# Optimization experiments

Measured on AMD Instinct MI355X. Metric: run time of the kernel, lower is better.

The kernel has to match this reference:

```python
import jax, jax.numpy as jnp
import numpy as np

B, L, DIM = 2, 2048, 2048
H, KV, HD = 32, 8, 64
N_REP = H // KV


def setup_inputs() -> dict:
    key = jax.random.key(0)
    ks = jax.random.split(key, 6)
    std = DIM ** -0.5
    std_o = (H * HD) ** -0.5 / np.sqrt(2 * 24)
    x = jax.random.normal(ks[0], (B, L, DIM), dtype=jnp.float32)
    # freqs_cis packs (cos, sin), each [L, head_dim//2]
    pos = jnp.arange(L, dtype=jnp.float32)[:, None]
    inv = 1.0 / (10000.0 ** (jnp.arange(0, HD, 2, dtype=jnp.float32) / HD))
    ang = pos * inv[None, :]
    freqs_cis = jnp.stack([jnp.cos(ang), jnp.sin(ang)], axis=0)
    wq = jax.random.normal(ks[1], (H * HD, DIM), dtype=jnp.float32) * std
    wk = jax.random.normal(ks[2], (KV * HD, DIM), dtype=jnp.float32) * std
    wv = jax.random.normal(ks[3], (KV * HD, DIM), dtype=jnp.float32) * std
    wo = jax.random.normal(ks[4], (DIM, H * HD), dtype=jnp.float32) * std_o
    return {"x": x, "freqs_cis": freqs_cis, "wq": wq, "wk": wk, "wv": wv, "wo": wo}


def _rope(t, cos, sin):
    # t: [B, L, h, HD]; interleaved (real, imag) pairs in last dim
    tr = t.reshape(*t.shape[:-1], HD // 2, 2)
    out_r = tr[..., 0] * cos - tr[..., 1] * sin
    out_i = tr[..., 0] * sin + tr[..., 1] * cos
    return jnp.stack([out_r, out_i], axis=-1).reshape(t.shape)


def reference(x, freqs_cis, wq, wk, wv, wo):
    Bb, Ll, _ = x.shape
    xq = (x @ wq.T).reshape(Bb, Ll, H, HD)
    xk = (x @ wk.T).reshape(Bb, Ll, KV, HD)
    xv = (x @ wv.T).reshape(Bb, Ll, KV, HD)
    cos = freqs_cis[0].reshape(1, Ll, 1, HD // 2)
    sin = freqs_cis[1].reshape(1, Ll, 1, HD // 2)
    xq = _rope(xq, cos, sin)
    xk = _rope(xk, cos, sin)
    # GQA: repeat_interleave kv heads to n_heads
    xk = jnp.repeat(xk, N_REP, axis=2)
    xv = jnp.repeat(xv, N_REP, axis=2)
    scale = 1.0 / jnp.sqrt(jnp.asarray(HD, x.dtype))
    scores = jnp.einsum('bihd,bjhd->bhij', xq, xk) * scale
    causal = jnp.tril(jnp.ones((Ll, Ll), dtype=bool))
    scores = jnp.where(causal[None, None], scores, jnp.finfo(scores.dtype).min)
    attn = jax.nn.softmax(scores, axis=-1)
    out = jnp.einsum('bhij,bjhd->bihd', attn, xv).reshape(Bb, Ll, H * HD)
    return out @ wo.T
```

## Files before the change

### kernel.cpp

```cpp
#include <hip/hip_runtime.h>
#include <stdint.h>

typedef __bf16 bf16;
typedef __attribute__((ext_vector_type(8))) __bf16 bf16x8;
typedef __attribute__((ext_vector_type(4))) __bf16 bf16x4;
typedef __attribute__((ext_vector_type(8))) short short8v;
typedef __attribute__((ext_vector_type(4))) short short4v;
typedef __attribute__((ext_vector_type(4))) float f32x4;

static constexpr int Bn = 2, Ln = 2048, DIMn = 2048, Hn = 32, KVn = 8, HDn = 64;
static constexpr int TS = 3072;

#if defined(__has_builtin)
#if __has_builtin(__builtin_amdgcn_exp2f)
#define EXP2(x) __builtin_amdgcn_exp2f(x)
#endif
#endif
#ifndef EXP2
#define EXP2(x) exp2f(x)
#endif

#define TO_LDS(p) ((__attribute__((address_space(3))) uint32_t*)(uintptr_t)(p))
#define TO_GLB(p) ((const __attribute__((address_space(1))) uint32_t*)(uintptr_t)(p))

__global__ void cast_all(const float* __restrict__ x, const float* __restrict__ wq,
                         const float* __restrict__ wk, const float* __restrict__ wv,
                         const float* __restrict__ wo, bf16* __restrict__ xb,
                         bf16* __restrict__ wqkvb, bf16* __restrict__ wob) {
    size_t i = (size_t)(blockIdx.x * blockDim.x + threadIdx.x) * 4;
    const float* src;
    bf16* dst;
    if (i < 8388608) {
        src = x + i; dst = xb + i;
    } else if (i < 8388608 + 6291456) {
        size_t j = i - 8388608;
        dst = wqkvb + j;
        if (j < 4194304)      src = wq + j;
        else if (j < 5242880) src = wk + (j - 4194304);
        else                  src = wv + (j - 5242880);
    } else {
        size_t j = i - 14680064;
        src = wo + j; dst = wob + j;
    }
    float4 v = *(const float4*)src;
    bf16 o[4] = {(bf16)v.x, (bf16)v.y, (bf16)v.z, (bf16)v.w};
    *(uint64_t*)dst = *(uint64_t*)o;
}

__global__ void rope_k(bf16* __restrict__ qkv, const float* __restrict__ fc) {
    int idx = blockIdx.x * blockDim.x + threadIdx.x;
    int i   = idx & 31;
    int kvh = (idx >> 5) & 7;
    int bl  = idx >> 8;
    int l   = bl & (Ln - 1);
    size_t base = (size_t)bl * TS + 2048 + kvh * 64 + 2 * i;
    float cr = fc[l * 32 + i];
    float sr = fc[65536 + l * 32 + i];
    float x0 = (float)qkv[base], x1 = (float)qkv[base + 1];
    qkv[base]     = (bf16)(x0 * cr - x1 * sr);
    qkv[base + 1] = (bf16)(x0 * sr + x1 * cr);
}

static __device__ __forceinline__ void barrier_f() {
    asm volatile("" ::: "memory");
    __builtin_amdgcn_s_barrier();
    asm volatile("" ::: "memory");
}

template <int N>
static __device__ __forceinline__ void waitcnt_vm() {
    if constexpr (N == 0) asm volatile("s_waitcnt vmcnt(0)" ::: "memory");
    else if constexpr (N == 6) asm volatile("s_waitcnt vmcnt(6)" ::: "memory");
    else if constexpr (N == 7) asm volatile("s_waitcnt vmcnt(7)" ::: "memory");
    else static_assert(N == 0 || N == 6 || N == 7, "add vmcnt literal");
}

template <int BM, int BN, bool OUT_BF16>
__global__ __launch_bounds__(512, 1) void gemm256(const bf16* __restrict__ A,
                                                  const bf16* __restrict__ Bm,
                                                  void* __restrict__ C,
                                                  int M, int N, int K) {
    (void)M;
    constexpr int MI = BM / 32;
    constexpr int NI = BN / 64;
    constexpr int MLO = MI / 2, MHI = MI - MLO;
    constexpr int NLO = NI / 2, NHI = NI - NLO;
    constexpr int AJ = BM / 64, BJ = BN / 64, LPT = AJ + BJ;
    __shared__ bf16 sA[2][BM * 64];
    __shared__ bf16 sB[2][BN * 64];
    const int t    = threadIdx.x;
    const int wave = t >> 6, lane = t & 63;
    const int q4 = lane >> 4, l16 = lane & 15;
    const int wm = wave >> 2, wn = wave & 3;
    const int r8l = lane >> 3;
    const int csw = ((lane & 7) ^ r8l) * 8;

    const size_t bm = (size_t)blockIdx.y * BM, bn = (size_t)blockIdx.x * BN;
    const bf16* pa = A  + (bm + (size_t)(wave * 8 + r8l)) * K + csw;
    const bf16* pb = Bm + (bn + (size_t)(wave * 8 + r8l)) * K + csw;
    const int NT = K >> 6;

#define STGA(buf, kt)                                                                          \
    _Pragma("unroll") for (int j = 0; j < AJ; ++j)                                             \
        __builtin_amdgcn_global_load_lds(TO_GLB(pa + (size_t)j * 64 * K + (size_t)(kt) * 64),  \
                                         TO_LDS(&sA[buf][(j * 64 + wave * 8) * 64]), 16, 0, 0)
#define STGB(buf, kt)                                                                          \
    _Pragma("unroll") for (int j = 0; j < BJ; ++j)                                             \
        __builtin_amdgcn_global_load_lds(TO_GLB(pb + (size_t)j * 64 * K + (size_t)(kt) * 64),  \
                                         TO_LDS(&sB[buf][(j * 64 + wave * 8) * 64]), 16, 0, 0)

#define RDA(mi_)                                                                               \
    _Pragma("unroll") for (int kk = 0; kk < 2; ++kk)                                           \
        af[mi_][kk] = *(const bf16x8*)(la + (wm * (BM / 2) + (mi_) * 16 + l16) * 64 +          \
                                       ((kk * 4 + q4) ^ sw) * 8)
#define RDB(ni_)                                                                               \
    _Pragma("unroll") for (int kk = 0; kk < 2; ++kk)                                           \
        bfr[ni_][kk] = *(const bf16x8*)(lb + (wn * (BN / 4) + (ni_) * 16 + l16) * 64 +         \
                                        ((kk * 4 + q4) ^ sw) * 8)

#define MMQ(m0, mc, n0, nc2)                                                                   \
    _Pragma("unroll") for (int mi = 0; mi < (mc); ++mi)                                        \
    _Pragma("unroll") for (int ni = 0; ni < (nc2); ++ni)                                       \
    _Pragma("unroll") for (int kk = 0; kk < 2; ++kk)                                           \
        acc[(m0) + mi][(n0) + ni] = __builtin_amdgcn_mfma_f32_16x16x32_bf16(                   \
            af[(m0) + mi][kk], bfr[(n0) + ni][kk], acc[(m0) + mi][(n0) + ni], 0, 0, 0)

    STGA(0, 0); STGB(0, 0);
    STGA(1, 1); STGB(1, 1);
    waitcnt_vm<LPT>();
    __builtin_amdgcn_s_barrier();
    asm volatile("" ::: "memory");

    f32x4 acc[MI][NI] = {};
    bf16x8 af[MI][2], bfr[NI][2];

    for (int k = 0; k < NT; ++k) {
        const int c = k & 1;
        const bf16* la = &sA[c][0];
        const bf16* lb = &sB[c][0];
        const int sw = (l16 & 7);

#pragma unroll
        for (int mi = 0; mi < MLO; ++mi) { RDA(mi); }
#pragma unroll
        for (int ni = 0; ni < NLO; ++ni) { RDB(ni); }
        barrier_f();
        __builtin_amdgcn_s_setprio(1);
        MMQ(0, MLO, 0, NLO);
        __builtin_amdgcn_s_setprio(0);
        barrier_f();

#pragma unroll
        for (int mi = MLO; mi < MI; ++mi) { RDA(mi); }
#pragma unroll
        for (int ni = NLO; ni < NI; ++ni) { RDB(ni); }
        barrier_f();
        __builtin_amdgcn_s_setprio(1);
        MMQ(MLO, MHI, NLO, NHI);
        __builtin_amdgcn_s_setprio(0);
        barrier_f();

        if (k + 2 < NT) { STGA(c, k + 2); }
        barrier_f();
        __builtin_amdgcn_s_setprio(1);
        MMQ(MLO, MHI, 0, NLO);
        __builtin_amdgcn_s_setprio(0);
        barrier_f();

        if (k + 2 < NT) {
            STGB(c, k + 2);
            waitcnt_vm<LPT>();
        } else if (k == NT - 2) {
            waitcnt_vm<0>();
        }
        barrier_f();
        __builtin_amdgcn_s_setprio(1);
        MMQ(0, MLO, NLO, NHI);
        __builtin_amdgcn_s_setprio(0);
        barrier_f();
    }
#undef STGA
#undef STGB
#undef RDA
#undef RDB
#undef MMQ

#pragma unroll
    for (int mi = 0; mi < MI; ++mi)
#pragma unroll
        for (int ni = 0; ni < NI; ++ni)
#pragma unroll
            for (int r = 0; r < 4; ++r) {
                size_t row = bm + wm * (BM / 2) + mi * 16 + q4 * 4 + r;
                size_t col = bn + wn * (BN / 4) + ni * 16 + l16;
                if (OUT_BF16)
                    ((bf16*)C)[row * (size_t)N + col] = (bf16)acc[mi][ni][r];
                else
                    ((float*)C)[row * (size_t)N + col] = acc[mi][ni][r];
            }
}

__global__ __launch_bounds__(256, 2) void attn_kernel(const bf16* __restrict__ QKV,
                                                      const float* __restrict__ fc,
                                                      bf16* __restrict__ O) {
    constexpr int LDK = 72;
    __shared__ bf16 sK[64 * LDK];
    __shared__ bf16 sV[64 * LDK];
    const int t    = threadIdx.x;
    const int wave = t >> 6, lane = t & 63;
    const int q4 = lane >> 4, l16 = lane & 15;
    const int hidx = wave & 1, qh = wave >> 1;
    const int L = blockIdx.x;
    const int qtile = 31 - (L >> 5);
    const int inner = L & 31;
    const int b = inner & 1, kvh = (inner >> 1) & 7, hp = (inner >> 4) & 1;
    const int h = kvh * 4 + hp * 2 + hidx;
    constexpr float SC = 0.125f * 1.44269504088896340736f;

    const bf16* kb = QKV + (size_t)(b * Ln) * TS + 2048 + kvh * 64;
    const bf16* vb = kb + 512;
    const int krow = t >> 3;
    const int kc8  = (t & 7) * 8;
    const int kp2  = (t & 31) * 2;
    const int vh8  = (t >> 5) * 8;

    bf16x8 qf[2][2];
#pragma unroll
    for (int g2 = 0; g2 < 2; ++g2) {
        int ql = qtile * 64 + (qh * 2 + g2) * 16 + l16;
        const bf16* qp = QKV + (size_t)(b * Ln + ql) * TS + h * 64;
#pragma unroll
        for (int hc = 0; hc < 2; ++hc) {
            bf16x8 raw = *(const bf16x8*)(qp + hc * 32 + q4 * 8);
            float4 c4 = *(const float4*)(fc + ql * 32 + hc * 16 + q4 * 4);
            float4 s4 = *(const float4*)(fc + 65536 + ql * 32 + hc * 16 + q4 * 4);
            bf16x8 o;
#pragma unroll
            for (int m = 0; m < 4; ++m) {
                float cr = ((const float*)&c4)[m], sr = ((const float*)&s4)[m];
                float x0 = (float)raw[2 * m], x1 = (float)raw[2 * m + 1];
                o[2 * m]     = (bf16)((x0 * cr - x1 * sr) * SC);
                o[2 * m + 1] = (bf16)((x0 * sr + x1 * cr) * SC);
            }
            qf[g2][hc] = o;
        }
    }

    f32x4 o_acc[2][4] = {};
    float l_r[2] = {0.f, 0.f};

    bf16x8 kreg[2], vrA, vrB;
#pragma unroll
    for (int p = 0; p < 2; ++p)
        kreg[p] = *(const bf16x8*)(kb + (size_t)(p * 32 + krow) * TS + kc8);
    vrA = *(const bf16x8*)(vb + (size_t)kp2 * TS + vh8);
    vrB = *(const bf16x8*)(vb + (size_t)(kp2 + 1) * TS + vh8);

    for (int kt = 0; kt <= qtile; ++kt) {
#pragma unroll
        for (int p = 0; p < 2; ++p)
            *(float4*)(&sK[(p * 32 + krow) * LDK + kc8]) = *(float4*)&kreg[p];
        {
            short8v sa = __builtin_bit_cast(short8v, vrA);
            short8v sb = __builtin_bit_cast(short8v, vrB);
#pragma unroll
            for (int j = 0; j < 8; ++j) {
                uint32_t d = (uint32_t)(uint16_t)sa[j] |
                             ((uint32_t)(uint16_t)sb[j] << 16);
                *(uint32_t*)(&sV[(vh8 + j) * LDK + kp2]) = d;
            }
        }
        __syncthreads();

        if (kt < qtile) {
#pragma unroll
            for (int p = 0; p < 2; ++p)
                kreg[p] = *(const bf16x8*)(kb + (size_t)((kt + 1) * 64 + p * 32 + krow) * TS + kc8);
            vrA = *(const bf16x8*)(vb + (size_t)((kt + 1) * 64 + kp2) * TS + vh8);
            vrB = *(const bf16x8*)(vb + (size_t)((kt + 1) * 64 + kp2 + 1) * TS + vh8);
        }

        bf16x8 kf[4][2];
#pragma unroll
        for (int c = 0; c < 4; ++c)
#pragma unroll
            for (int hc = 0; hc < 2; ++hc)
                kf[c][hc] = *(const bf16x8*)(&sK[(c * 16 + l16) * LDK + hc * 32 + q4 * 8]);
        short4v vf[4][4];
#pragma unroll
        for (int nc = 0; nc < 4; ++nc)
#pragma unroll
            for (int c = 0; c < 4; ++c)
                vf[nc][c] = *(const short4v*)(&sV[(nc * 16 + l16) * LDK + c * 16 + q4 * 4]);

        const bool diag = (kt == qtile);
#pragma unroll
        for (int g2 = 0; g2 < 2; ++g2) {
            f32x4 s[4];
            __builtin_amdgcn_s_setprio(1);
#pragma unroll
            for (int c = 0; c < 4; ++c) {
                f32x4 a = {};
                a = __builtin_amdgcn_mfma_f32_16x16x32_bf16(kf[c][0], qf[g2][0], a, 0, 0, 0);
                a = __builtin_amdgcn_mfma_f32_16x16x32_bf16(kf[c][1], qf[g2][1], a, 0, 0, 0);
                s[c] = a;
            }
            __builtin_amdgcn_s_setprio(0);
            int qrow = qtile * 64 + (qh * 2 + g2) * 16 + l16;
            float lsum = 0.f;
            short4v pb4[4];
            if (diag) {
#pragma unroll
                for (int c = 0; c < 4; ++c) {
                    float pc[4];
#pragma unroll
                    for (int r = 0; r < 4; ++r) {
                        float p = EXP2(s[c][r] - 12.f);
                        if (kt * 64 + c * 16 + q4 * 4 + r > qrow) p = 0.f;
                        pc[r] = p;
                        bf16 ph = (bf16)p;
                        pb4[c][r] = *(const short*)&ph;
                    }
                    lsum += (pc[0] + pc[1]) + (pc[2] + pc[3]);
                }
            } else {
#pragma unroll
                for (int c = 0; c < 4; ++c) {
                    float pc[4];
#pragma unroll
                    for (int r = 0; r < 4; ++r) {
                        float p = EXP2(s[c][r] - 12.f);
                        pc[r] = p;
                        bf16 ph = (bf16)p;
                        pb4[c][r] = *(const short*)&ph;
                    }
                    lsum += (pc[0] + pc[1]) + (pc[2] + pc[3]);
                }
            }
            l_r[g2] += lsum;
            __builtin_amdgcn_s_setprio(1);
#pragma unroll
            for (int nc = 0; nc < 4; ++nc)
#pragma unroll
                for (int c = 0; c < 4; ++c)
                    o_acc[g2][nc] = __builtin_amdgcn_mfma_f32_16x16x16bf16_1k(
                        vf[nc][c], pb4[c], o_acc[g2][nc], 0, 0, 0);
            __builtin_amdgcn_s_setprio(0);
        }
        __syncthreads();
    }

#pragma unroll
    for (int g2 = 0; g2 < 2; ++g2) {
        float l = l_r[g2];
        l += __shfl_xor(l, 16, 64);
        l += __shfl_xor(l, 32, 64);
        float inv = 1.f / l;
        int qrow = qtile * 64 + (qh * 2 + g2) * 16 + l16;
        bf16* op = O + (size_t)(b * Ln + qrow) * (Hn * HDn) + h * 64;
#pragma unroll
        for (int nc = 0; nc < 4; ++nc) {
            bf16x4 o;
#pragma unroll
            for (int r = 0; r < 4; ++r) o[r] = (bf16)(o_acc[g2][nc][r] * inv);
            *(bf16x4*)(op + nc * 16 + q4 * 4) = o;
        }
    }
}

extern "C" void kernel_launch(void* const* d_in, const int* in_sizes, int n_in,
                              void* d_out, int out_size, void* d_ws, size_t ws_size,
                              hipStream_t stream) {
    const float* x  = (const float*)d_in[0];
    const float* fc = (const float*)d_in[1];
    const float* wq = (const float*)d_in[2];
    const float* wk = (const float*)d_in[3];
    const float* wv = (const float*)d_in[4];
    const float* wo = (const float*)d_in[5];
    float* out = (float*)d_out;

    const size_t T = (size_t)Bn * Ln;
    char* p = (char*)d_ws;
    bf16* xb    = (bf16*)p; p += T * DIMn * 2;
    bf16* wqkvb = (bf16*)p; p += (size_t)TS * DIMn * 2;
    bf16* wob   = (bf16*)p; p += (size_t)DIMn * Hn * HDn * 2;
    bf16* qkv   = (bf16*)p; p += T * TS * 2;
    bf16* ao    = (bf16*)p; p += T * Hn * HDn * 2;

    cast_all<<<dim3(18432), dim3(256), 0, stream>>>(x, wq, wk, wv, wo, xb, wqkvb, wob);

    gemm256<256, 192, true><<<dim3(TS / 192, 4096 / 256), dim3(512), 0, stream>>>(
        xb, wqkvb, qkv, 4096, TS, 2048);

    rope_k<<<dim3(4096), dim3(256), 0, stream>>>(qkv, fc);

    attn_kernel<<<dim3(1024), dim3(256), 0, stream>>>(qkv, fc, ao);

    gemm256<128, 256, false><<<dim3(2048 / 256, 4096 / 128), dim3(512), 0, stream>>>(
        ao, wob, out, 4096, 2048, 2048);
}
```

Baseline: 279.2 us.

## Use 256x256 split-LDS GEMM and pair causal query tiles in attention

Replaces the parameterized GEMM with a fixed 256x256 tile kernel. It splits the A and B shared tiles into halves so half of the next k-step is prefetched earlier, and it raises launch bounds to allow 2 blocks per CU. The attention kernel now processes two query tiles per block (tile i and 31-i), which balances causal work and halves the grid. The larger tiles cut grid counts for both GEMMs (192 and 128 blocks), which risks poor CU utilization. They also raise register and LDS pressure: 128KB LDS per block may prevent 2 blocks per CU.

```diff
diff --git a/kernel.cpp b/kernel.cpp
--- a/kernel.cpp
+++ b/kernel.cpp
@@ -70,24 +70,18 @@
 template <int N>
 static __device__ __forceinline__ void waitcnt_vm() {
     if constexpr (N == 0) asm volatile("s_waitcnt vmcnt(0)" ::: "memory");
-    else if constexpr (N == 6) asm volatile("s_waitcnt vmcnt(6)" ::: "memory");
-    else if constexpr (N == 7) asm volatile("s_waitcnt vmcnt(7)" ::: "memory");
-    else static_assert(N == 0 || N == 6 || N == 7, "add vmcnt literal");
-}
-
-template <int BM, int BN, bool OUT_BF16>
-__global__ __launch_bounds__(512, 1) void gemm256(const bf16* __restrict__ A,
-                                                  const bf16* __restrict__ Bm,
-                                                  void* __restrict__ C,
-                                                  int M, int N, int K) {
+    else if constexpr (N == 4) asm volatile("s_waitcnt vmcnt(4)" ::: "memory");
+    else static_assert(N == 0 || N == 4, "add vmcnt literal");
+}
+
+template <bool OUT_BF16>
+__global__ __launch_bounds__(512, 2) void gemm8p(const bf16* __restrict__ A,
+                                                 const bf16* __restrict__ Bm,
+                                                 void* __restrict__ C,
+                                                 int M, int N, int K) {
     (void)M;
-    constexpr int MI = BM / 32;
-    constexpr int NI = BN / 64;
-    constexpr int MLO = MI / 2, MHI = MI - MLO;
-    constexpr int NLO = NI / 2, NHI = NI - NLO;
-    constexpr int AJ = BM / 64, BJ = BN / 64, LPT = AJ + BJ;
-    __shared__ bf16 sA[2][BM * 64];
-    __shared__ bf16 sB[2][BN * 64];
+    __shared__ bf16 sA[2][2][128 * 64];
+    __shared__ bf16 sB[2][2][128 * 64];
     const int t    = threadIdx.x;
     const int wave = t >> 6, lane = t & 63;
     const int q4 = lane >> 4, l16 = lane & 15;
@@ -95,104 +89,105 @@
     const int r8l = lane >> 3;
     const int csw = ((lane & 7) ^ r8l) * 8;
 
-    const size_t bm = (size_t)blockIdx.y * BM, bn = (size_t)blockIdx.x * BN;
+    const size_t bm = (size_t)blockIdx.y * 256, bn = (size_t)blockIdx.x * 256;
     const bf16* pa = A  + (bm + (size_t)(wave * 8 + r8l)) * K + csw;
     const bf16* pb = Bm + (bn + (size_t)(wave * 8 + r8l)) * K + csw;
     const int NT = K >> 6;
 
-#define STGA(buf, kt)                                                                          \
-    _Pragma("unroll") for (int j = 0; j < AJ; ++j)                                             \
-        __builtin_amdgcn_global_load_lds(TO_GLB(pa + (size_t)j * 64 * K + (size_t)(kt) * 64),  \
-                                         TO_LDS(&sA[buf][(j * 64 + wave * 8) * 64]), 16, 0, 0)
-#define STGB(buf, kt)                                                                          \
-    _Pragma("unroll") for (int j = 0; j < BJ; ++j)                                             \
-        __builtin_amdgcn_global_load_lds(TO_GLB(pb + (size_t)j * 64 * K + (size_t)(kt) * 64),  \
-                                         TO_LDS(&sB[buf][(j * 64 + wave * 8) * 64]), 16, 0, 0)
-
-#define RDA(mi_)                                                                               \
+#define STG_A(buf, h, kt)                                                                      \
+    _Pragma("unroll") for (int j = 0; j < 2; ++j)                                              \
+        __builtin_amdgcn_global_load_lds(                                                      \
+            TO_GLB(pa + (size_t)((h) * 128 + j * 64) * K + (size_t)(kt) * 64),                 \
+            TO_LDS(&sA[buf][h][(j * 64 + wave * 8) * 64]), 16, 0, 0)
+#define STG_B(buf, h, kt)                                                                      \
+    _Pragma("unroll") for (int j = 0; j < 2; ++j)                                              \
+        __builtin_amdgcn_global_load_lds(                                                      \
+            TO_GLB(pb + (size_t)((h) * 128 + j * 64) * K + (size_t)(kt) * 64),                 \
+            TO_LDS(&sB[buf][h][(j * 64 + wave * 8) * 64]), 16, 0, 0)
+
+#define RD_A(mi_)                                                                              \
     _Pragma("unroll") for (int kk = 0; kk < 2; ++kk)                                           \
-        af[mi_][kk] = *(const bf16x8*)(la + (wm * (BM / 2) + (mi_) * 16 + l16) * 64 +          \
-                                       ((kk * 4 + q4) ^ sw) * 8)
-#define RDB(ni_)                                                                               \
+        af[mi_][kk] = *(const bf16x8*)(&sA[c][wm][((mi_) * 16 + l16) * 64 +                    \
+                                                  (((kk * 4 + q4) ^ sw) * 8)])
+#define RD_B(ni_)                                                                              \
     _Pragma("unroll") for (int kk = 0; kk < 2; ++kk)                                           \
-        bfr[ni_][kk] = *(const bf16x8*)(lb + (wn * (BN / 4) + (ni_) * 16 + l16) * 64 +         \
-                                        ((kk * 4 + q4) ^ sw) * 8)
-
-#define MMQ(m0, mc, n0, nc2)                                                                   \
-    _Pragma("unroll") for (int mi = 0; mi < (mc); ++mi)                                        \
-    _Pragma("unroll") for (int ni = 0; ni < (nc2); ++ni)                                       \
+        bfr[ni_][kk] = *(const bf16x8*)(&sB[c][wn >> 1][((wn & 1) * 64 + (ni_) * 16 + l16) * 64 + \
+                                                        (((kk * 4 + q4) ^ sw) * 8)])
+
+#define MMQ(qm, qn)                                                                            \
+    _Pragma("unroll") for (int mi = 0; mi < 4; ++mi)                                           \
+    _Pragma("unroll") for (int ni = 0; ni < 2; ++ni)                                           \
     _Pragma("unroll") for (int kk = 0; kk < 2; ++kk)                                           \
-        acc[(m0) + mi][(n0) + ni] = __builtin_amdgcn_mfma_f32_16x16x32_bf16(                   \
-            af[(m0) + mi][kk], bfr[(n0) + ni][kk], acc[(m0) + mi][(n0) + ni], 0, 0, 0)
-
-    STGA(0, 0); STGB(0, 0);
-    STGA(1, 1); STGB(1, 1);
-    waitcnt_vm<LPT>();
+        acc[(qm) * 4 + mi][(qn) * 2 + ni] = __builtin_amdgcn_mfma_f32_16x16x32_bf16(           \
+            af[(qm) * 4 + mi][kk], bfr[(qn) * 2 + ni][kk],                                     \
+            acc[(qm) * 4 + mi][(qn) * 2 + ni], 0, 0, 0)
+
+    STG_A(0, 0, 0); STG_A(0, 1, 0); STG_B(0, 0, 0); STG_B(0, 1, 0);
+    STG_A(1, 0, 1); STG_B(1, 0, 1);
+    waitcnt_vm<4>();
     __builtin_amdgcn_s_barrier();
     asm volatile("" ::: "memory");
 
-    f32x4 acc[MI][NI] = {};
-    bf16x8 af[MI][2], bfr[NI][2];
+    f32x4 acc[8][4] = {};
+    bf16x8 af[8][2], bfr[4][2];
 
     for (int k = 0; k < NT; ++k) {
         const int c = k & 1;
-        const bf16* la = &sA[c][0];
-        const bf16* lb = &sB[c][0];
-        const int sw = (l16 & 7);
-
-#pragma unroll
-        for (int mi = 0; mi < MLO; ++mi) { RDA(mi); }
-#pragma unroll
-        for (int ni = 0; ni < NLO; ++ni) { RDB(ni); }
+        const int sw = l16 & 7;
+
+        RD_A(0); RD_A(1); RD_A(2); RD_A(3);
+        RD_B(0); RD_B(1);
+        if (k + 1 < NT) { STG_A(c ^ 1, 1, k + 1); }
+        asm volatile("s_waitcnt lgkmcnt(8)" ::: "memory");
         barrier_f();
         __builtin_amdgcn_s_setprio(1);
-        MMQ(0, MLO, 0, NLO);
+        MMQ(0, 0);
         __builtin_amdgcn_s_setprio(0);
         barrier_f();
 
-#pragma unroll
-        for (int mi = MLO; mi < MI; ++mi) { RDA(mi); }
-#pragma unroll
-        for (int ni = NLO; ni < NI; ++ni) { RDB(ni); }
+        RD_A(4); RD_A(5); RD_A(6); RD_A(7);
+        RD_B(2); RD_B(3);
+        if (k + 1 < NT) { STG_B(c ^ 1, 1, k + 1); }
+        asm volatile("s_waitcnt lgkmcnt(8)" ::: "memory");
         barrier_f();
         __builtin_amdgcn_s_setprio(1);
-        MMQ(MLO, MHI, NLO, NHI);
+        MMQ(1, 1);
         __builtin_amdgcn_s_setprio(0);
         barrier_f();
 
-        if (k + 2 < NT) { STGA(c, k + 2); }
+        if (k + 2 < NT) { STG_A(c, 0, k + 2); }
         barrier_f();
         __builtin_amdgcn_s_setprio(1);
-        MMQ(MLO, MHI, 0, NLO);
+        MMQ(1, 0);
         __builtin_amdgcn_s_setprio(0);
         barrier_f();
 
         if (k + 2 < NT) {
-            STGB(c, k + 2);
-            waitcnt_vm<LPT>();
+            STG_B(c, 0, k + 2);
+            waitcnt_vm<4>();
         } else if (k == NT - 2) {
             waitcnt_vm<0>();
         }
         barrier_f();
         __builtin_amdgcn_s_setprio(1);
-        MMQ(0, MLO, NLO, NHI);
+        MMQ(0, 1);
         __builtin_amdgcn_s_setprio(0);
         barrier_f();
     }
-#undef STGA
-#undef STGB
-#undef RDA
-#undef RDB
+#undef STG_A
+#undef STG_B
+#undef RD_A
+#undef RD_B
 #undef MMQ
 
 #pragma unroll
-    for (int mi = 0; mi < MI; ++mi)
-#pragma unroll
-        for (int ni = 0; ni < NI; ++ni)
+    for (int mi = 0; mi < 8; ++mi)
+#pragma unroll
+        for (int ni = 0; ni < 4; ++ni)
 #pragma unroll
             for (int r = 0; r < 4; ++r) {
-                size_t row = bm + wm * (BM / 2) + mi * 16 + q4 * 4 + r;
-                size_t col = bn + wn * (BN / 4) + ni * 16 + l16;
+                size_t row = bm + wm * 128 + mi * 16 + q4 * 4 + r;
+                size_t col = bn + wn * 64 + ni * 16 + l16;
                 if (OUT_BF16)
                     ((bf16*)C)[row * (size_t)N + col] = (bf16)acc[mi][ni][r];
                 else
@@ -211,9 +206,7 @@
     const int q4 = lane >> 4, l16 = lane & 15;
     const int hidx = wave & 1, qh = wave >> 1;
     const int L = blockIdx.x;
-    const int qtile = 31 - (L >> 5);
-    const int inner = L & 31;
-    const int b = inner & 1, kvh = (inner >> 1) & 7, hp = (inner >> 4) & 1;
+    const int pair = L & 15, hp = (L >> 4) & 1, kvh = (L >> 5) & 7, b = L >> 8;
     const int h = kvh * 4 + hp * 2 + hidx;
     constexpr float SC = 0.125f * 1.44269504088896340736f;
 
@@ -224,146 +217,150 @@
     const int kp2  = (t & 31) * 2;
     const int vh8  = (t >> 5) * 8;
 
-    bf16x8 qf[2][2];
-#pragma unroll
-    for (int g2 = 0; g2 < 2; ++g2) {
-        int ql = qtile * 64 + (qh * 2 + g2) * 16 + l16;
-        const bf16* qp = QKV + (size_t)(b * Ln + ql) * TS + h * 64;
-#pragma unroll
-        for (int hc = 0; hc < 2; ++hc) {
-            bf16x8 raw = *(const bf16x8*)(qp + hc * 32 + q4 * 8);
-            float4 c4 = *(const float4*)(fc + ql * 32 + hc * 16 + q4 * 4);
-            float4 s4 = *(const float4*)(fc + 65536 + ql * 32 + hc * 16 + q4 * 4);
-            bf16x8 o;
-#pragma unroll
-            for (int m = 0; m < 4; ++m) {
-                float cr = ((const float*)&c4)[m], sr = ((const float*)&s4)[m];
-                float x0 = (float)raw[2 * m], x1 = (float)raw[2 * m + 1];
-                o[2 * m]     = (bf16)((x0 * cr - x1 * sr) * SC);
-                o[2 * m + 1] = (bf16)((x0 * sr + x1 * cr) * SC);
-            }
-            qf[g2][hc] = o;
+    for (int half = 0; half < 2; ++half) {
+        const int qtile = half == 0 ? 31 - pair : pair;
+
+        bf16x8 qf[2][2];
+#pragma unroll
+        for (int g2 = 0; g2 < 2; ++g2) {
+            int ql = qtile * 64 + (qh * 2 + g2) * 16 + l16;
+            const bf16* qp = QKV + (size_t)(b * Ln + ql) * TS + h * 64;
+#pragma unroll
+            for (int hc = 0; hc < 2; ++hc) {
+                bf16x8 raw = *(const bf16x8*)(qp + hc * 32 + q4 * 8);
+                float4 c4 = *(const float4*)(fc + ql * 32 + hc * 16 + q4 * 4);
+                float4 s4 = *(const float4*)(fc + 65536 + ql * 32 + hc * 16 + q4 * 4);
+                bf16x8 o;
+#pragma unroll
+                for (int m = 0; m < 4; ++m) {
+                    float cr = ((const float*)&c4)[m], sr = ((const float*)&s4)[m];
+                    float x0 = (float)raw[2 * m], x1 = (float)raw[2 * m + 1];
+                    o[2 * m]     = (bf16)((x0 * cr - x1 * sr) * SC);
+                    o[2 * m + 1] = (bf16)((x0 * sr + x1 * cr) * SC);
+                }
+                qf[g2][hc] = o;
+            }
         }
-    }
-
-    f32x4 o_acc[2][4] = {};
-    float l_r[2] = {0.f, 0.f};
-
-    bf16x8 kreg[2], vrA, vrB;
-#pragma unroll
-    for (int p = 0; p < 2; ++p)
-        kreg[p] = *(const bf16x8*)(kb + (size_t)(p * 32 + krow) * TS + kc8);
-    vrA = *(const bf16x8*)(vb + (size_t)kp2 * TS + vh8);
-    vrB = *(const bf16x8*)(vb + (size_t)(kp2 + 1) * TS + vh8);
-
-    for (int kt = 0; kt <= qtile; ++kt) {
+
+        f32x4 o_acc[2][4] = {};
+        float l_r[2] = {0.f, 0.f};
+
+        bf16x8 kreg[2], vrA, vrB;
 #pragma unroll
         for (int p = 0; p < 2; ++p)
-            *(float4*)(&sK[(p * 32 + krow) * LDK + kc8]) = *(float4*)&kreg[p];
-        {
-            short8v sa = __builtin_bit_cast(short8v, vrA);
-            short8v sb = __builtin_bit_cast(short8v, vrB);
-#pragma unroll
-            for (int j = 0; j < 8; ++j) {
-                uint32_t d = (uint32_t)(uint16_t)sa[j] |
-                             ((uint32_t)(uint16_t)sb[j] << 16);
-                *(uint32_t*)(&sV[(vh8 + j) * LDK + kp2]) = d;
-            }
+            kreg[p] = *(const bf16x8*)(kb + (size_t)(p * 32 + krow) * TS + kc8);
+        vrA = *(const bf16x8*)(vb + (size_t)kp2 * TS + vh8);
+        vrB = *(const bf16x8*)(vb + (size_t)(kp2 + 1) * TS + vh8);
+
+        for (int kt = 0; kt <= qtile; ++kt) {
+#pragma unroll
+            for (int p = 0; p < 2; ++p)
+                *(float4*)(&sK[(p * 32 + krow) * LDK + kc8]) = *(float4*)&kreg[p];
+            {
+                short8v sa = __builtin_bit_cast(short8v, vrA);
+                short8v sb = __builtin_bit_cast(short8v, vrB);
+#pragma unroll
+                for (int j = 0; j < 8; ++j) {
+                    uint32_t d = (uint32_t)(uint16_t)sa[j] |
+                                 ((uint32_t)(uint16_t)sb[j] << 16);
+                    *(uint32_t*)(&sV[(vh8 + j) * LDK + kp2]) = d;
+                }
+            }
+            __syncthreads();
+
+            if (kt < qtile) {
+#pragma unroll
+                for (int p = 0; p < 2; ++p)
+                    kreg[p] = *(const bf16x8*)(kb + (size_t)((kt + 1) * 64 + p * 32 + krow) * TS + kc8);
+                vrA = *(const bf16x8*)(vb + (size_t)((kt + 1) * 64 + kp2) * TS + vh8);
+                vrB = *(const bf16x8*)(vb + (size_t)((kt + 1) * 64 + kp2 + 1) * TS + vh8);
+            }
+
+            bf16x8 kf[4][2];
+#pragma unroll
+            for (int c = 0; c < 4; ++c)
+#pragma unroll
+                for (int hc = 0; hc < 2; ++hc)
+                    kf[c][hc] = *(const bf16x8*)(&sK[(c * 16 + l16) * LDK + hc * 32 + q4 * 8]);
+            short4v vf[4][4];
+#pragma unroll
+            for (int nc = 0; nc < 4; ++nc)
+#pragma unroll
+                for (int c = 0; c < 4; ++c)
+                    vf[nc][c] = *(const short4v*)(&sV[(nc * 16 + l16) * LDK + c * 16 + q4 * 4]);
+
+            const bool diag = (kt == qtile);
+#pragma unroll
+            for (int g2 = 0; g2 < 2; ++g2) {
+                f32x4 s[4];
+                __builtin_amdgcn_s_setprio(1);
+#pragma unroll
+                for (int c = 0; c < 4; ++c) {
+                    f32x4 a = {};
+                    a = __builtin_amdgcn_mfma_f32_16x16x32_bf16(kf[c][0], qf[g2][0], a, 0, 0, 0);
+                    a = __builtin_amdgcn_mfma_f32_16x16x32_bf16(kf[c][1], qf[g2][1], a, 0, 0, 0);
+                    s[c] = a;
+                }
+                __builtin_amdgcn_s_setprio(0);
+                int qrow = qtile * 64 + (qh * 2 + g2) * 16 + l16;
+                float lsum = 0.f;
+                short4v pb4[4];
+                if (diag) {
+#pragma unroll
+                    for (int c = 0; c < 4; ++c) {
+                        float pc[4];
+#pragma unroll
+                        for (int r = 0; r < 4; ++r) {
+                            float p = EXP2(s[c][r] - 12.f);
+                            if (kt * 64 + c * 16 + q4 * 4 + r > qrow) p = 0.f;
+                            pc[r] = p;
+                            bf16 ph = (bf16)p;
+                            pb4[c][r] = *(const short*)&ph;
+                        }
+                        lsum += (pc[0] + pc[1]) + (pc[2] + pc[3]);
+                    }
+                } else {
+#pragma unroll
+                    for (int c = 0; c < 4; ++c) {
+                        float pc[4];
+#pragma unroll
+                        for (int r = 0; r < 4; ++r) {
+                            float p = EXP2(s[c][r] - 12.f);
+                            pc[r] = p;
+                            bf16 ph = (bf16)p;
+                            pb4[c][r] = *(const short*)&ph;
+                        }
+                        lsum += (pc[0] + pc[1]) + (pc[2] + pc[3]);
+                    }
+                }
+                l_r[g2] += lsum;
+                __builtin_amdgcn_s_setprio(1);
+#pragma unroll
+                for (int nc = 0; nc < 4; ++nc)
+#pragma unroll
+                    for (int c = 0; c < 4; ++c)
+                        o_acc[g2][nc] = __builtin_amdgcn_mfma_f32_16x16x16bf16_1k(
+                            vf[nc][c], pb4[c], o_acc[g2][nc], 0, 0, 0);
+                __builtin_amdgcn_s_setprio(0);
+            }
+            __syncthreads();
         }
-        __syncthreads();
-
-        if (kt < qtile) {
-#pragma unroll
-            for (int p = 0; p < 2; ++p)
-                kreg[p] = *(const bf16x8*)(kb + (size_t)((kt + 1) * 64 + p * 32 + krow) * TS + kc8);
-            vrA = *(const bf16x8*)(vb + (size_t)((kt + 1) * 64 + kp2) * TS + vh8);
-            vrB = *(const bf16x8*)(vb + (size_t)((kt + 1) * 64 + kp2 + 1) * TS + vh8);
-        }
-
-        bf16x8 kf[4][2];
-#pragma unroll
-        for (int c = 0; c < 4; ++c)
-#pragma unroll
-            for (int hc = 0; hc < 2; ++hc)
-                kf[c][hc] = *(const bf16x8*)(&sK[(c * 16 + l16) * LDK + hc * 32 + q4 * 8]);
-        short4v vf[4][4];
-#pragma unroll
-        for (int nc = 0; nc < 4; ++nc)
-#pragma unroll
-            for (int c = 0; c < 4; ++c)
-                vf[nc][c] = *(const short4v*)(&sV[(nc * 16 + l16) * LDK + c * 16 + q4 * 4]);
-
-        const bool diag = (kt == qtile);
+
 #pragma unroll
         for (int g2 = 0; g2 < 2; ++g2) {
-            f32x4 s[4];
-            __builtin_amdgcn_s_setprio(1);
-#pragma unroll
-            for (int c = 0; c < 4; ++c) {
-                f32x4 a = {};
-                a = __builtin_amdgcn_mfma_f32_16x16x32_bf16(kf[c][0], qf[g2][0], a, 0, 0, 0);
-                a = __builtin_amdgcn_mfma_f32_16x16x32_bf16(kf[c][1], qf[g2][1], a, 0, 0, 0);
-                s[c] = a;
-            }
-            __builtin_amdgcn_s_setprio(0);
+            float l = l_r[g2];
+            l += __shfl_xor(l, 16, 64);
+            l += __shfl_xor(l, 32, 64);
+            float inv = 1.f / l;
             int qrow = qtile * 64 + (qh * 2 + g2) * 16 + l16;
-            float lsum = 0.f;
-            short4v pb4[4];
-            if (diag) {
-#pragma unroll
-                for (int c = 0; c < 4; ++c) {
-                    float pc[4];
-#pragma unroll
-                    for (int r = 0; r < 4; ++r) {
-                        float p = EXP2(s[c][r] - 12.f);
-                        if (kt * 64 + c * 16 + q4 * 4 + r > qrow) p = 0.f;
-                        pc[r] = p;
-                        bf16 ph = (bf16)p;
-                        pb4[c][r] = *(const short*)&ph;
-                    }
-                    lsum += (pc[0] + pc[1]) + (pc[2] + pc[3]);
-                }
-            } else {
-#pragma unroll
-                for (int c = 0; c < 4; ++c) {
-                    float pc[4];
-#pragma unroll
-                    for (int r = 0; r < 4; ++r) {
-                        float p = EXP2(s[c][r] - 12.f);
-                        pc[r] = p;
-                        bf16 ph = (bf16)p;
-                        pb4[c][r] = *(const short*)&ph;
-                    }
-                    lsum += (pc[0] + pc[1]) + (pc[2] + pc[3]);
-                }
-            }
-            l_r[g2] += lsum;
-            __builtin_amdgcn_s_setprio(1);
-#pragma unroll
-            for (int nc = 0; nc < 4; ++nc)
-#pragma unroll
-                for (int c = 0; c < 4; ++c)
-                    o_acc[g2][nc] = __builtin_amdgcn_mfma_f32_16x16x16bf16_1k(
-                        vf[nc][c], pb4[c], o_acc[g2][nc], 0, 0, 0);
-            __builtin_amdgcn_s_setprio(0);
-        }
-        __syncthreads();
-    }
-
-#pragma unroll
-    for (int g2 = 0; g2 < 2; ++g2) {
-        float l = l_r[g2];
-        l += __shfl_xor(l, 16, 64);
-        l += __shfl_xor(l, 32, 64);
-        float inv = 1.f / l;
-        int qrow = qtile * 64 + (qh * 2 + g2) * 16 + l16;
-        bf16* op = O + (size_t)(b * Ln + qrow) * (Hn * HDn) + h * 64;
-#pragma unroll
-        for (int nc = 0; nc < 4; ++nc) {
-            bf16x4 o;
-#pragma unroll
-            for (int r = 0; r < 4; ++r) o[r] = (bf16)(o_acc[g2][nc][r] * inv);
-            *(bf16x4*)(op + nc * 16 + q4 * 4) = o;
+            bf16* op = O + (size_t)(b * Ln + qrow) * (Hn * HDn) + h * 64;
+#pragma unroll
+            for (int nc = 0; nc < 4; ++nc) {
+                bf16x4 o;
+#pragma unroll
+                for (int r = 0; r < 4; ++r) o[r] = (bf16)(o_acc[g2][nc][r] * inv);
+                *(bf16x4*)(op + nc * 16 + q4 * 4) = o;
+            }
         }
     }
 }
@@ -389,13 +386,13 @@
 
     cast_all<<<dim3(18432), dim3(256), 0, stream>>>(x, wq, wk, wv, wo, xb, wqkvb, wob);
 
-    gemm256<256, 192, true><<<dim3(TS / 192, 4096 / 256), dim3(512), 0, stream>>>(
+    gemm8p<true><<<dim3(TS / 256, 4096 / 256), dim3(512), 0, stream>>>(
         xb, wqkvb, qkv, 4096, TS, 2048);
 
     rope_k<<<dim3(4096), dim3(256), 0, stream>>>(qkv, fc);
 
-    attn_kernel<<<dim3(1024), dim3(256), 0, stream>>>(qkv, fc, ao);
-
-    gemm256<128, 256, false><<<dim3(2048 / 256, 4096 / 128), dim3(512), 0, stream>>>(
+    attn_kernel<<<dim3(512), dim3(256), 0, stream>>>(qkv, fc, ao);
+
+    gemm8p<false><<<dim3(2048 / 256, 4096 / 256), dim3(512), 0, stream>>>(
         ao, wob, out, 4096, 2048, 2048);
 }
```

Measured after the change: 299.5 us. +7.3%, slower.
